# Kernel tuning notes

Hardware: AMD Instinct MI355X
Metric: run time of the kernel (lower is better)

## Reference

```python
import jax, jax.numpy as jnp
import numpy as np

N_NODES, N_EDGES, MAX_NB = 40000, 80000, 4
INPUT_SIZE, NODE_FDIM, HIDDEN = 384, 256, 256
DEPTH = 6


def setup_inputs() -> dict:
    key = jax.random.key(0)
    ks = jax.random.split(key, 16)
    s = 0.05  # weight init scale
    return {
        "fnode": jax.random.normal(ks[0], (N_NODES, NODE_FDIM), dtype=jnp.float32),
        "fmess": jax.random.normal(ks[1], (N_EDGES, INPUT_SIZE), dtype=jnp.float32),
        "agraph": jax.random.randint(ks[2], (N_NODES, MAX_NB), 0, N_EDGES),
        "bgraph": jax.random.randint(ks[3], (N_EDGES, MAX_NB), 0, N_EDGES),
        "mask": jnp.ones((N_NODES, 1), dtype=jnp.float32),
        "Wz": jax.random.normal(ks[4], (INPUT_SIZE + HIDDEN, HIDDEN), dtype=jnp.float32) * s,
        "bz": jnp.zeros((HIDDEN,), dtype=jnp.float32),
        "Wr": jax.random.normal(ks[5], (INPUT_SIZE, HIDDEN), dtype=jnp.float32) * s,
        "Ur": jax.random.normal(ks[6], (HIDDEN, HIDDEN), dtype=jnp.float32) * s,
        "bur": jnp.zeros((HIDDEN,), dtype=jnp.float32),
        "Wh": jax.random.normal(ks[7], (INPUT_SIZE + HIDDEN, HIDDEN), dtype=jnp.float32) * s,
        "bh": jnp.zeros((HIDDEN,), dtype=jnp.float32),
        "Wo": jax.random.normal(ks[8], (NODE_FDIM + HIDDEN, HIDDEN), dtype=jnp.float32) * s,
        "bo": jnp.zeros((HIDDEN,), dtype=jnp.float32),
        "depth": DEPTH,
    }


def reference(fnode, fmess, agraph, bgraph, mask, Wz, bz, Wr, Ur, bur, Wh, bh, Wo, bo, depth):
    E, H = fmess.shape[0], Wz.shape[1]
    # message 0 is padding -> kept at zero each step (mask[0,0]=0 in torch GRU)
    msg_mask = jnp.ones((E, 1), dtype=fmess.dtype).at[0, 0].set(0.0)
    rx = fmess @ Wr  # precomputable: [E, H], reset gate input term

    def step(h, _):
        h_nei = h[bgraph]                      # [E, nb, H] gather
        sum_h = h_nei.sum(axis=1)              # [E, H]
        z = jax.nn.sigmoid(jnp.concatenate([fmess, sum_h], axis=1) @ Wz + bz)
        r = jax.nn.sigmoid(rx[:, None, :] + h_nei @ Ur + bur)  # [E, nb, H]
        sum_gh = (r * h_nei).sum(axis=1)
        pre_h = jnp.tanh(jnp.concatenate([fmess, sum_gh], axis=1) @ Wh + bh)
        h_new = ((1.0 - z) * sum_h + z * pre_h) * msg_mask
        return h_new, None

    h0 = jnp.zeros((E, H), dtype=fmess.dtype)
    h, _ = jax.lax.scan(step, h0, None, length=depth)

    nei_message = h[agraph].sum(axis=1)        # [N, H] gather-sum over incoming edges
    node_hiddens = jax.nn.relu(jnp.concatenate([fnode, nei_message], axis=1) @ Wo + bo)
    return node_hiddens * mask, h
```

## Files before the change

kernel.cpp:

```cpp
#include <hip/hip_runtime.h>
#include <stdint.h>

#define N_NODES 40000
#define N_EDGES 80000
#define HID 256
#define DEPTH_FIXED 6
#define NPAD 40064

typedef __bf16 bf16;
typedef __bf16 bf16x4 __attribute__((ext_vector_type(4)));
typedef __bf16 bf16x8 __attribute__((ext_vector_type(8)));
typedef float f32x4 __attribute__((ext_vector_type(4)));

#define TPAD 136

__device__ __forceinline__ float sigmoidf_(float x) { return 1.f / (1.f + __expf(-x)); }
__device__ __forceinline__ float tanhf_(float x) { float e = __expf(2.f * x); return 1.f - 2.f / (e + 1.f); }

__device__ __forceinline__ void gld_lds16(const void* g, void* l) {
    __builtin_amdgcn_global_load_lds(
        (const __attribute__((address_space(1))) uint32_t*)g,
        (__attribute__((address_space(3))) uint32_t*)l, 16, 0, 0);
}

__device__ __forceinline__ void stage_tile(const bf16* __restrict__ src, int ld, int r0, int k0,
                                           bf16* lds, int tid) {
#pragma unroll
    for (int jj = 0; jj < 2; ++jj) {
        int s = jj * 256 + tid;
        int c = s ^ ((s >> 3) & 3);
        gld_lds16(src + (size_t)(r0 + (c >> 2)) * ld + k0 + (c & 3) * 8, lds + s * 8);
    }
}

__device__ __forceinline__ void mfma_tile(const bf16* lds_a, const bf16* lds_b,
                                          int wm, int wn, int lane, f32x4 (&acc)[4][4]) {
    const int li = lane & 15, quad = lane >> 4;
    const int sw = quad ^ ((li >> 1) & 3);
    bf16x8 a[4], b[4];
#pragma unroll
    for (int i = 0; i < 4; ++i)
        a[i] = *(const bf16x8*)(lds_a + ((wm * 64 + i * 16 + li) * 4 + sw) * 8);
#pragma unroll
    for (int j = 0; j < 4; ++j)
        b[j] = *(const bf16x8*)(lds_b + ((wn * 64 + j * 16 + li) * 4 + sw) * 8);
#pragma unroll
    for (int i = 0; i < 4; ++i)
#pragma unroll
        for (int j = 0; j < 4; ++j)
            acc[i][j] = __builtin_amdgcn_mfma_f32_16x16x32_bf16(a[i], b[j], acc[i][j], 0, 0, 0);
}

__global__ __launch_bounds__(256) void gemm_single_k(
    const bf16* __restrict__ A, const bf16* __restrict__ BT,
    const float* __restrict__ bias, bf16* __restrict__ C, int K, int ldc) {
    __shared__ __align__(16) char smem[34816];
    bf16* sA = (bf16*)smem;
    bf16* sB = sA + 4096;
    const int tid = threadIdx.x, lane = tid & 63, wave = tid >> 6;
    const int wm = wave >> 1, wn = wave & 1;
    const int m0 = blockIdx.x * 128, n0 = blockIdx.y * 128;
    f32x4 acc[4][4] = {};
    for (int k0 = 0; k0 < K; k0 += 32) {
        stage_tile(A, K, m0, k0, sA, tid);
        stage_tile(BT, K, n0, k0, sB, tid);
        __syncthreads();
        mfma_tile(sA, sB, wm, wn, lane, acc);
        __syncthreads();
    }
    bf16* tC = (bf16*)smem;
#pragma unroll
    for (int i = 0; i < 4; ++i)
#pragma unroll
        for (int j = 0; j < 4; ++j) {
            const int col = wn * 64 + j * 16 + (lane & 15);
#pragma unroll
            for (int r = 0; r < 4; ++r) {
                const int lr = wm * 64 + i * 16 + (lane >> 4) * 4 + r;
                tC[lr * TPAD + col] = (bf16)acc[i][j][r];
            }
        }
    __syncthreads();
#pragma unroll
    for (int s = 0; s < 8; ++s) {
        int v = s * 256 + tid;
        int lr = v >> 4, c8 = (v & 15) * 8;
        bf16x8 cv = *(const bf16x8*)(tC + lr * TPAD + c8);
        bf16x8 o;
        if (bias) {
            float4 b0 = *(const float4*)(bias + n0 + c8);
            float4 b1 = *(const float4*)(bias + n0 + c8 + 4);
            o[0] = (bf16)((float)cv[0] + b0.x); o[1] = (bf16)((float)cv[1] + b0.y);
            o[2] = (bf16)((float)cv[2] + b0.z); o[3] = (bf16)((float)cv[3] + b0.w);
            o[4] = (bf16)((float)cv[4] + b1.x); o[5] = (bf16)((float)cv[5] + b1.y);
            o[6] = (bf16)((float)cv[6] + b1.z); o[7] = (bf16)((float)cv[7] + b1.w);
        } else {
            o = cv;
        }
        *(bf16x8*)(C + (size_t)(m0 + lr) * ldc + n0 + c8) = o;
    }
}

__global__ __launch_bounds__(256) void gemm_gru_k(
    const bf16* __restrict__ A1, const bf16* __restrict__ A2,
    const bf16* __restrict__ B1T, const bf16* __restrict__ B2T,
    const bf16* __restrict__ P, bf16* __restrict__ H, float* __restrict__ HF) {
    __shared__ __align__(16) char smem[34816];
    bf16* s0 = (bf16*)smem;
    bf16* s1 = s0 + 4096;
    bf16* s2 = s1 + 4096;
    bf16* s3 = s2 + 4096;
    const int tid = threadIdx.x, lane = tid & 63, wave = tid >> 6;
    const int wm = wave >> 1, wn = wave & 1;
    const int m0 = blockIdx.x * 128, n0 = blockIdx.y * 128;
    f32x4 acc1[4][4] = {}, acc2[4][4] = {};
    for (int k0 = 0; k0 < 256; k0 += 32) {
        stage_tile(A1, 256, m0, k0, s0, tid);
        stage_tile(B1T, 256, n0, k0, s1, tid);
        stage_tile(A2, 256, m0, k0, s2, tid);
        stage_tile(B2T, 256, n0, k0, s3, tid);
        __syncthreads();
        mfma_tile(s0, s1, wm, wn, lane, acc1);
        mfma_tile(s2, s3, wm, wn, lane, acc2);
        __syncthreads();
    }
    bf16* tZ = (bf16*)smem;
    bf16* tH = tZ + 64 * TPAD;
#pragma unroll
    for (int pass = 0; pass < 2; ++pass) {
        if (wm == pass) {
#pragma unroll
            for (int i = 0; i < 4; ++i)
#pragma unroll
                for (int j = 0; j < 4; ++j) {
                    const int col = wn * 64 + j * 16 + (lane & 15);
#pragma unroll
                    for (int r = 0; r < 4; ++r) {
                        const int lr = i * 16 + (lane >> 4) * 4 + r;
                        tZ[lr * TPAD + col] = (bf16)acc1[i][j][r];
                        tH[lr * TPAD + col] = (bf16)acc2[i][j][r];
                    }
                }
        }
        __syncthreads();
#pragma unroll
        for (int s = 0; s < 4; ++s) {
            int v = s * 256 + tid;
            int lr = v >> 4, c8 = (v & 15) * 8;
            int grow = m0 + pass * 64 + lr;
            int gcol = n0 + c8;
            bf16x8 zl = *(const bf16x8*)(tZ + lr * TPAD + c8);
            bf16x8 hl = *(const bf16x8*)(tH + lr * TPAD + c8);
            bf16x8 zx = *(const bf16x8*)(P + (size_t)grow * 768 + 256 + gcol);
            bf16x8 hx = *(const bf16x8*)(P + (size_t)grow * 768 + 512 + gcol);
            bf16x8 sh = *(const bf16x8*)(A1 + (size_t)grow * 256 + gcol);
            bf16x8 o;
            float of[8];
#pragma unroll
            for (int r = 0; r < 8; ++r) {
                float z = sigmoidf_((float)zl[r] + (float)zx[r]);
                float p = tanhf_((float)hl[r] + (float)hx[r]);
                float hn = (1.f - z) * (float)sh[r] + z * p;
                if (grow == 0) hn = 0.f;
                o[r] = (bf16)hn;
                of[r] = hn;
            }
            *(bf16x8*)(H + (size_t)grow * 256 + gcol) = o;
            if (HF) {
                *(float4*)(HF + (size_t)grow * 256 + gcol) = make_float4(of[0], of[1], of[2], of[3]);
                *(float4*)(HF + (size_t)grow * 256 + gcol + 4) = make_float4(of[4], of[5], of[6], of[7]);
            }
        }
        __syncthreads();
    }
}

__global__ __launch_bounds__(256) void gemm_out_k(
    const bf16* __restrict__ A1, const bf16* __restrict__ A2,
    const bf16* __restrict__ B1T, const bf16* __restrict__ B2T,
    const float* __restrict__ bo, const float* __restrict__ mask, float* __restrict__ out) {
    __shared__ __align__(16) char smem[34816];
    bf16* s0 = (bf16*)smem;
    bf16* s1 = s0 + 4096;
    bf16* s2 = s1 + 4096;
    bf16* s3 = s2 + 4096;
    const int tid = threadIdx.x, lane = tid & 63, wave = tid >> 6;
    const int wm = wave >> 1, wn = wave & 1;
    const int m0 = blockIdx.x * 128, n0 = blockIdx.y * 128;
    f32x4 acc1[4][4] = {}, acc2[4][4] = {};
    for (int k0 = 0; k0 < 256; k0 += 32) {
        stage_tile(A1, 256, m0, k0, s0, tid);
        stage_tile(B1T, 256, n0, k0, s1, tid);
        stage_tile(A2, 256, m0, k0, s2, tid);
        stage_tile(B2T, 256, n0, k0, s3, tid);
        __syncthreads();
        mfma_tile(s0, s1, wm, wn, lane, acc1);
        mfma_tile(s2, s3, wm, wn, lane, acc2);
        __syncthreads();
    }
    bf16* tC = (bf16*)smem;
#pragma unroll
    for (int i = 0; i < 4; ++i)
#pragma unroll
        for (int j = 0; j < 4; ++j) {
            const int col = wn * 64 + j * 16 + (lane & 15);
#pragma unroll
            for (int r = 0; r < 4; ++r) {
                const int lr = wm * 64 + i * 16 + (lane >> 4) * 4 + r;
                tC[lr * TPAD + col] = (bf16)(acc1[i][j][r] + acc2[i][j][r]);
            }
        }
    __syncthreads();
#pragma unroll
    for (int s = 0; s < 8; ++s) {
        int v = s * 256 + tid;
        int lr = v >> 4, c8 = (v & 15) * 8;
        int grow = m0 + lr;
        if (grow >= N_NODES) continue;
        int gcol = n0 + c8;
        bf16x8 cv = *(const bf16x8*)(tC + lr * TPAD + c8);
        float4 b0 = *(const float4*)(bo + gcol);
        float4 b1 = *(const float4*)(bo + gcol + 4);
        float mk = mask[grow];
        float4 o0, o1;
        o0.x = fmaxf((float)cv[0] + b0.x, 0.f) * mk;
        o0.y = fmaxf((float)cv[1] + b0.y, 0.f) * mk;
        o0.z = fmaxf((float)cv[2] + b0.z, 0.f) * mk;
        o0.w = fmaxf((float)cv[3] + b0.w, 0.f) * mk;
        o1.x = fmaxf((float)cv[4] + b1.x, 0.f) * mk;
        o1.y = fmaxf((float)cv[5] + b1.y, 0.f) * mk;
        o1.z = fmaxf((float)cv[6] + b1.z, 0.f) * mk;
        o1.w = fmaxf((float)cv[7] + b1.w, 0.f) * mk;
        *(float4*)(out + (size_t)grow * 256 + gcol) = o0;
        *(float4*)(out + (size_t)grow * 256 + gcol + 4) = o1;
    }
}

__global__ __launch_bounds__(256) void gather_gru_k(
    const int* __restrict__ bgraph, const bf16* __restrict__ H, const bf16* __restrict__ HU,
    const bf16* __restrict__ P, bf16* __restrict__ sumH, bf16* __restrict__ sumGH) {
    int i = blockIdx.x * 256 + threadIdx.x;
    int e = i >> 5, c8 = (i & 31) * 8;
    int4 nb = *(const int4*)(bgraph + (size_t)e * 4);
    bf16x8 rx = *(const bf16x8*)(P + (size_t)e * 768 + c8);
    int bi[4] = {nb.x, nb.y, nb.z, nb.w};
    float sh[8] = {}, gh[8] = {};
#pragma unroll
    for (int j = 0; j < 4; ++j) {
        bf16x8 hv = *(const bf16x8*)(H + (size_t)bi[j] * HID + c8);
        bf16x8 uv = *(const bf16x8*)(HU + (size_t)bi[j] * HID + c8);
#pragma unroll
        for (int r = 0; r < 8; ++r) {
            float hf = (float)hv[r];
            float rr = sigmoidf_((float)rx[r] + (float)uv[r]);
            sh[r] += hf;
            gh[r] += rr * hf;
        }
    }
    bf16x8 os, og;
#pragma unroll
    for (int r = 0; r < 8; ++r) { os[r] = (bf16)sh[r]; og[r] = (bf16)gh[r]; }
    *(bf16x8*)(sumH + (size_t)e * HID + c8) = os;
    *(bf16x8*)(sumGH + (size_t)e * HID + c8) = og;
}

__global__ __launch_bounds__(256) void gather_nei_k(
    const int* __restrict__ agraph, const bf16* __restrict__ H, bf16* __restrict__ nei) {
    int i = blockIdx.x * 256 + threadIdx.x;
    int v = i >> 5, c8 = (i & 31) * 8;
    bf16x8 o;
    if (v < N_NODES) {
        int4 nb = *(const int4*)(agraph + (size_t)v * 4);
        int bi[4] = {nb.x, nb.y, nb.z, nb.w};
        float s[8] = {};
#pragma unroll
        for (int j = 0; j < 4; ++j) {
            bf16x8 hv = *(const bf16x8*)(H + (size_t)bi[j] * HID + c8);
#pragma unroll
            for (int r = 0; r < 8; ++r) s[r] += (float)hv[r];
        }
#pragma unroll
        for (int r = 0; r < 8; ++r) o[r] = (bf16)s[r];
    } else {
#pragma unroll
        for (int r = 0; r < 8; ++r) o[r] = (bf16)0.f;
    }
    *(bf16x8*)(nei + (size_t)v * HID + c8) = o;
}

__global__ __launch_bounds__(256) void step1_k(const bf16* __restrict__ P, bf16* __restrict__ H) {
    int i = blockIdx.x * 256 + threadIdx.x;
    int e = i >> 5, c8 = (i & 31) * 8;
    bf16x8 zx = *(const bf16x8*)(P + (size_t)e * 768 + 256 + c8);
    bf16x8 hx = *(const bf16x8*)(P + (size_t)e * 768 + 512 + c8);
    bf16x8 o;
#pragma unroll
    for (int r = 0; r < 8; ++r) {
        float h = sigmoidf_((float)zx[r]) * tanhf_((float)hx[r]);
        if (e == 0) h = 0.f;
        o[r] = (bf16)h;
    }
    *(bf16x8*)(H + (size_t)e * HID + c8) = o;
}

__global__ void cvt_bf16_k(const float* __restrict__ src, bf16* __restrict__ dst, int n4) {
    int i = blockIdx.x * 256 + threadIdx.x;
    if (i >= n4) return;
    float4 v = ((const float4*)src)[i];
    bf16x4 o = {(bf16)v.x, (bf16)v.y, (bf16)v.z, (bf16)v.w};
    *((bf16x4*)dst + i) = o;
}

__global__ void cvt_fnode_k(const float* __restrict__ src, bf16* __restrict__ dst) {
    int i = blockIdx.x * 256 + threadIdx.x;
    int row = i >> 6;
    bf16x4 o = {(bf16)0.f, (bf16)0.f, (bf16)0.f, (bf16)0.f};
    if (row < N_NODES) {
        float4 v = ((const float4*)src)[i];
        o[0] = (bf16)v.x; o[1] = (bf16)v.y; o[2] = (bf16)v.z; o[3] = (bf16)v.w;
    }
    *((bf16x4*)dst + i) = o;
}

__global__ void prep_wpre_k(const float* __restrict__ Wr, const float* __restrict__ Wz,
                            const float* __restrict__ Wh, bf16* __restrict__ WT) {
    int idx = blockIdx.x * 256 + threadIdx.x;
    if (idx >= 768 * 384) return;
    int n = idx / 384, k = idx % 384;
    float v;
    if (n < 256) v = Wr[(size_t)k * 256 + n];
    else if (n < 512) v = Wz[(size_t)k * 256 + (n - 256)];
    else v = Wh[(size_t)k * 256 + (n - 512)];
    WT[idx] = (bf16)v;
}

__global__ void prep_bias_k(const float* __restrict__ bur, const float* __restrict__ bz,
                            const float* __restrict__ bh, float* __restrict__ bp) {
    int n = blockIdx.x * 256 + threadIdx.x;
    if (n >= 768) return;
    bp[n] = n < 256 ? bur[n] : (n < 512 ? bz[n - 256] : bh[n - 512]);
}

__global__ void prep_t256_k(const float* __restrict__ W, bf16* __restrict__ T, int roff) {
    int idx = blockIdx.x * 256 + threadIdx.x;
    int n = idx >> 8, k = idx & 255;
    T[idx] = (bf16)W[(size_t)(roff + k) * 256 + n];
}

extern "C" void kernel_launch(void* const* d_in, const int* in_sizes, int n_in,
                              void* d_out, int out_size, void* d_ws, size_t ws_size,
                              hipStream_t stream) {
    (void)in_sizes; (void)n_in; (void)out_size; (void)ws_size;
    const float* fnode = (const float*)d_in[0];
    const float* fmess = (const float*)d_in[1];
    const int* agraph = (const int*)d_in[2];
    const int* bgraph = (const int*)d_in[3];
    const float* mask = (const float*)d_in[4];
    const float* Wz = (const float*)d_in[5];
    const float* bz = (const float*)d_in[6];
    const float* Wr = (const float*)d_in[7];
    const float* Ur = (const float*)d_in[8];
    const float* bur = (const float*)d_in[9];
    const float* Wh = (const float*)d_in[10];
    const float* bh = (const float*)d_in[11];
    const float* Wo = (const float*)d_in[12];
    const float* bo = (const float*)d_in[13];
    float* out_node = (float*)d_out;
    float* out_h = out_node + (size_t)N_NODES * HID;

    char* ws = (char*)d_ws;
    size_t off = 0;
    auto alloc = [&](size_t b) -> char* { char* p = ws + off; off += (b + 255) & ~(size_t)255; return p; };
    bf16* P     = (bf16*)alloc((size_t)N_EDGES * 768 * 2);
    bf16* Hb    = (bf16*)alloc((size_t)N_EDGES * HID * 2);
    bf16* HU    = (bf16*)alloc((size_t)N_EDGES * HID * 2);
    bf16* sumH  = (bf16*)alloc((size_t)N_EDGES * HID * 2);
    bf16* sumGH = (bf16*)alloc((size_t)N_EDGES * HID * 2);
    bf16* fnodeB= (bf16*)alloc((size_t)NPAD * HID * 2);
    bf16* nei   = (bf16*)alloc((size_t)NPAD * HID * 2);
    bf16* WTpre = (bf16*)alloc((size_t)768 * 384 * 2);
    bf16* UrT   = (bf16*)alloc(65536 * 2);
    bf16* WzBT  = (bf16*)alloc(65536 * 2);
    bf16* WhBT  = (bf16*)alloc(65536 * 2);
    bf16* WoTT  = (bf16*)alloc(65536 * 2);
    bf16* WoBT  = (bf16*)alloc(65536 * 2);
    float* biasP= (float*)alloc(768 * 4);
    bf16* fmessB = sumH;

    cvt_bf16_k<<<30000, 256, 0, stream>>>(fmess, fmessB, N_EDGES * 384 / 4);
    cvt_fnode_k<<<NPAD * 64 / 256, 256, 0, stream>>>(fnode, fnodeB);
    prep_wpre_k<<<(768 * 384 + 255) / 256, 256, 0, stream>>>(Wr, Wz, Wh, WTpre);
    prep_bias_k<<<3, 256, 0, stream>>>(bur, bz, bh, biasP);
    prep_t256_k<<<256, 256, 0, stream>>>(Ur, UrT, 0);
    prep_t256_k<<<256, 256, 0, stream>>>(Wz, WzBT, 384);
    prep_t256_k<<<256, 256, 0, stream>>>(Wh, WhBT, 384);
    prep_t256_k<<<256, 256, 0, stream>>>(Wo, WoTT, 0);
    prep_t256_k<<<256, 256, 0, stream>>>(Wo, WoBT, 256);

    gemm_single_k<<<dim3(625, 6), 256, 0, stream>>>(fmessB, WTpre, biasP, P, 384, 768);

    step1_k<<<N_EDGES * 32 / 256, 256, 0, stream>>>(P, Hb);

    for (int d = 2; d <= DEPTH_FIXED; ++d) {
        gemm_single_k<<<dim3(625, 2), 256, 0, stream>>>(Hb, UrT, nullptr, HU, 256, 256);
        gather_gru_k<<<N_EDGES * 32 / 256, 256, 0, stream>>>(bgraph, Hb, HU, P, sumH, sumGH);
        gemm_gru_k<<<dim3(625, 2), 256, 0, stream>>>(sumH, sumGH, WzBT, WhBT, P, Hb,
                                                     d == DEPTH_FIXED ? out_h : nullptr);
    }

    gather_nei_k<<<NPAD * 32 / 256, 256, 0, stream>>>(agraph, Hb, nei);
    gemm_out_k<<<dim3(313, 2), 256, 0, stream>>>(fnodeB, nei, WoTT, WoBT, bo, mask, out_node);
}
```

Baseline: 1.478 ms.

## Fuse neighbor gather-GRU with Z/H gate GEMM into one per-step kernel

Replaces the separate gather_gru kernel and the gate GEMM with one kernel that gathers neighbor messages for a 32-edge tile, keeps sum_h and gated sum in LDS, and runs both 256-wide GEMMs plus the GRU epilogue before writing the new hidden state. This removes the global write and re-read of the sumH/sumGH intermediates and one launch per step. To avoid read/write races it double-buffers the hidden state. The cost is a small M tile (32 rows), so every block restages the full weight matrices from global/L2, and the MFMA work per weight load is lower.

```diff
diff --git a/kernel.cpp b/kernel.cpp
--- a/kernel.cpp
+++ b/kernel.cpp
@@ -6,6 +6,7 @@
 #define HID 256
 #define DEPTH_FIXED 6
 #define NPAD 40064
+#define MT 32
 
 typedef __bf16 bf16;
 typedef __bf16 bf16x4 __attribute__((ext_vector_type(4)));
@@ -13,6 +14,7 @@
 typedef float f32x4 __attribute__((ext_vector_type(4)));
 
 #define TPAD 136
+#define APAD 264
 
 __device__ __forceinline__ float sigmoidf_(float x) { return 1.f / (1.f + __expf(-x)); }
 __device__ __forceinline__ float tanhf_(float x) { float e = __expf(2.f * x); return 1.f - 2.f / (e + 1.f); }
@@ -49,6 +51,132 @@
 #pragma unroll
         for (int j = 0; j < 4; ++j)
             acc[i][j] = __builtin_amdgcn_mfma_f32_16x16x32_bf16(a[i], b[j], acc[i][j], 0, 0, 0);
+}
+
+__global__ __launch_bounds__(256, 3) void step_fused_k(
+    const int* __restrict__ bgraph, const bf16* __restrict__ Hcur,
+    const bf16* __restrict__ HU, const bf16* __restrict__ P,
+    const bf16* __restrict__ B1T, const bf16* __restrict__ B2T,
+    bf16* __restrict__ Hnew, float* __restrict__ HF) {
+    __shared__ __align__(16) bf16 sA1[MT * APAD];
+    __shared__ __align__(16) bf16 sA2[MT * APAD];
+    __shared__ __align__(16) bf16 sBst[256 * 32];
+    const int tid = threadIdx.x, lane = tid & 63, wave = tid >> 6;
+    const int m0 = blockIdx.x * MT;
+
+    {
+        const int r = tid >> 3, qc = tid & 7;
+        const int e = m0 + r;
+        const int4 nb = *(const int4*)(bgraph + (size_t)e * 4);
+        const int bi[4] = {nb.x, nb.y, nb.z, nb.w};
+        const bf16* prx = P + (size_t)e * 768 + qc * 32;
+        bf16x8 rx[4];
+#pragma unroll
+        for (int c = 0; c < 4; ++c) rx[c] = *(const bf16x8*)(prx + c * 8);
+        float sh[4][8] = {}, gh[4][8] = {};
+#pragma unroll
+        for (int j = 0; j < 4; ++j) {
+            const bf16* hp = Hcur + (size_t)bi[j] * HID + qc * 32;
+            const bf16* up = HU + (size_t)bi[j] * HID + qc * 32;
+            bf16x8 hv[4], uv[4];
+#pragma unroll
+            for (int c = 0; c < 4; ++c) { hv[c] = *(const bf16x8*)(hp + c * 8); uv[c] = *(const bf16x8*)(up + c * 8); }
+#pragma unroll
+            for (int c = 0; c < 4; ++c)
+#pragma unroll
+                for (int u = 0; u < 8; ++u) {
+                    float hf = (float)hv[c][u];
+                    float rr = sigmoidf_((float)rx[c][u] + (float)uv[c][u]);
+                    sh[c][u] += hf;
+                    gh[c][u] += rr * hf;
+                }
+        }
+#pragma unroll
+        for (int c = 0; c < 4; ++c) {
+            bf16x8 os, og;
+#pragma unroll
+            for (int u = 0; u < 8; ++u) { os[u] = (bf16)sh[c][u]; og[u] = (bf16)gh[c][u]; }
+            *(bf16x8*)(sA1 + r * APAD + qc * 32 + c * 8) = os;
+            *(bf16x8*)(sA2 + r * APAD + qc * 32 + c * 8) = og;
+        }
+    }
+    __syncthreads();
+
+    const int li = lane & 15, quad = lane >> 4;
+    const int sw = quad ^ ((li >> 1) & 3);
+    f32x4 accZ[2][4] = {}, accH[2][4] = {};
+#pragma unroll
+    for (int pass = 0; pass < 2; ++pass) {
+        const bf16* BT = pass ? B2T : B1T;
+        const bf16* sA = pass ? sA2 : sA1;
+        for (int t = 0; t < 8; ++t) {
+#pragma unroll
+            for (int jj = 0; jj < 4; ++jj) {
+                int s = jj * 256 + tid;
+                int c = s ^ ((s >> 3) & 3);
+                gld_lds16(BT + (size_t)(c >> 2) * 256 + t * 32 + (c & 3) * 8, sBst + s * 8);
+            }
+            __syncthreads();
+            bf16x8 a[2], b[4];
+#pragma unroll
+            for (int i = 0; i < 2; ++i)
+                a[i] = *(const bf16x8*)(sA + (i * 16 + li) * APAD + t * 32 + quad * 8);
+#pragma unroll
+            for (int j = 0; j < 4; ++j)
+                b[j] = *(const bf16x8*)(sBst + ((wave * 64 + j * 16 + li) * 4 + sw) * 8);
+#pragma unroll
+            for (int i = 0; i < 2; ++i)
+#pragma unroll
+                for (int j = 0; j < 4; ++j) {
+                    if (pass == 0) accZ[i][j] = __builtin_amdgcn_mfma_f32_16x16x32_bf16(a[i], b[j], accZ[i][j], 0, 0, 0);
+                    else           accH[i][j] = __builtin_amdgcn_mfma_f32_16x16x32_bf16(a[i], b[j], accH[i][j], 0, 0, 0);
+                }
+            __syncthreads();
+        }
+    }
+
+    bf16* tZ = sA2;
+    bf16* tH = sBst;
+#pragma unroll
+    for (int i = 0; i < 2; ++i)
+#pragma unroll
+        for (int j = 0; j < 4; ++j) {
+            const int col = wave * 64 + j * 16 + li;
+#pragma unroll
+            for (int r = 0; r < 4; ++r) {
+                const int row = i * 16 + quad * 4 + r;
+                tZ[row * APAD + col] = (bf16)accZ[i][j][r];
+                tH[row * 256 + col] = (bf16)accH[i][j][r];
+            }
+        }
+    __syncthreads();
+#pragma unroll
+    for (int s = 0; s < 4; ++s) {
+        int v = s * 256 + tid;
+        int lr = v >> 5, c8 = (v & 31) * 8;
+        int e = m0 + lr;
+        bf16x8 zl = *(const bf16x8*)(tZ + lr * APAD + c8);
+        bf16x8 hl = *(const bf16x8*)(tH + lr * 256 + c8);
+        bf16x8 shv = *(const bf16x8*)(sA1 + lr * APAD + c8);
+        bf16x8 zx = *(const bf16x8*)(P + (size_t)e * 768 + 256 + c8);
+        bf16x8 hx = *(const bf16x8*)(P + (size_t)e * 768 + 512 + c8);
+        bf16x8 o;
+        float of[8];
+#pragma unroll
+        for (int u = 0; u < 8; ++u) {
+            float z = sigmoidf_((float)zl[u] + (float)zx[u]);
+            float p = tanhf_((float)hl[u] + (float)hx[u]);
+            float hn = (1.f - z) * (float)shv[u] + z * p;
+            if (e == 0) hn = 0.f;
+            o[u] = (bf16)hn;
+            of[u] = hn;
+        }
+        *(bf16x8*)(Hnew + (size_t)e * HID + c8) = o;
+        if (HF) {
+            *(float4*)(HF + (size_t)e * HID + c8) = make_float4(of[0], of[1], of[2], of[3]);
+            *(float4*)(HF + (size_t)e * HID + c8 + 4) = make_float4(of[4], of[5], of[6], of[7]);
+        }
+    }
 }
 
 __global__ __launch_bounds__(256) void gemm_single_k(
@@ -98,80 +226,6 @@
             o = cv;
         }
         *(bf16x8*)(C + (size_t)(m0 + lr) * ldc + n0 + c8) = o;
-    }
-}
-
-__global__ __launch_bounds__(256) void gemm_gru_k(
-    const bf16* __restrict__ A1, const bf16* __restrict__ A2,
-    const bf16* __restrict__ B1T, const bf16* __restrict__ B2T,
-    const bf16* __restrict__ P, bf16* __restrict__ H, float* __restrict__ HF) {
-    __shared__ __align__(16) char smem[34816];
-    bf16* s0 = (bf16*)smem;
-    bf16* s1 = s0 + 4096;
-    bf16* s2 = s1 + 4096;
-    bf16* s3 = s2 + 4096;
-    const int tid = threadIdx.x, lane = tid & 63, wave = tid >> 6;
-    const int wm = wave >> 1, wn = wave & 1;
-    const int m0 = blockIdx.x * 128, n0 = blockIdx.y * 128;
-    f32x4 acc1[4][4] = {}, acc2[4][4] = {};
-    for (int k0 = 0; k0 < 256; k0 += 32) {
-        stage_tile(A1, 256, m0, k0, s0, tid);
-        stage_tile(B1T, 256, n0, k0, s1, tid);
-        stage_tile(A2, 256, m0, k0, s2, tid);
-        stage_tile(B2T, 256, n0, k0, s3, tid);
-        __syncthreads();
-        mfma_tile(s0, s1, wm, wn, lane, acc1);
-        mfma_tile(s2, s3, wm, wn, lane, acc2);
-        __syncthreads();
-    }
-    bf16* tZ = (bf16*)smem;
-    bf16* tH = tZ + 64 * TPAD;
-#pragma unroll
-    for (int pass = 0; pass < 2; ++pass) {
-        if (wm == pass) {
-#pragma unroll
-            for (int i = 0; i < 4; ++i)
-#pragma unroll
-                for (int j = 0; j < 4; ++j) {
-                    const int col = wn * 64 + j * 16 + (lane & 15);
-#pragma unroll
-                    for (int r = 0; r < 4; ++r) {
-                        const int lr = i * 16 + (lane >> 4) * 4 + r;
-                        tZ[lr * TPAD + col] = (bf16)acc1[i][j][r];
-                        tH[lr * TPAD + col] = (bf16)acc2[i][j][r];
-                    }
-                }
-        }
-        __syncthreads();
-#pragma unroll
-        for (int s = 0; s < 4; ++s) {
-            int v = s * 256 + tid;
-            int lr = v >> 4, c8 = (v & 15) * 8;
-            int grow = m0 + pass * 64 + lr;
-            int gcol = n0 + c8;
-            bf16x8 zl = *(const bf16x8*)(tZ + lr * TPAD + c8);
-            bf16x8 hl = *(const bf16x8*)(tH + lr * TPAD + c8);
-            bf16x8 zx = *(const bf16x8*)(P + (size_t)grow * 768 + 256 + gcol);
-            bf16x8 hx = *(const bf16x8*)(P + (size_t)grow * 768 + 512 + gcol);
-            bf16x8 sh = *(const bf16x8*)(A1 + (size_t)grow * 256 + gcol);
-            bf16x8 o;
-            float of[8];
-#pragma unroll
-            for (int r = 0; r < 8; ++r) {
-                float z = sigmoidf_((float)zl[r] + (float)zx[r]);
-                float p = tanhf_((float)hl[r] + (float)hx[r]);
-                float hn = (1.f - z) * (float)sh[r] + z * p;
-                if (grow == 0) hn = 0.f;
-                o[r] = (bf16)hn;
-                of[r] = hn;
-            }
-            *(bf16x8*)(H + (size_t)grow * 256 + gcol) = o;
-            if (HF) {
-                *(float4*)(HF + (size_t)grow * 256 + gcol) = make_float4(of[0], of[1], of[2], of[3]);
-                *(float4*)(HF + (size_t)grow * 256 + gcol + 4) = make_float4(of[4], of[5], of[6], of[7]);
-            }
-        }
-        __syncthreads();
     }
 }
 
@@ -236,34 +290,6 @@
     }
 }
 
-__global__ __launch_bounds__(256) void gather_gru_k(
-    const int* __restrict__ bgraph, const bf16* __restrict__ H, const bf16* __restrict__ HU,
-    const bf16* __restrict__ P, bf16* __restrict__ sumH, bf16* __restrict__ sumGH) {
-    int i = blockIdx.x * 256 + threadIdx.x;
-    int e = i >> 5, c8 = (i & 31) * 8;
-    int4 nb = *(const int4*)(bgraph + (size_t)e * 4);
-    bf16x8 rx = *(const bf16x8*)(P + (size_t)e * 768 + c8);
-    int bi[4] = {nb.x, nb.y, nb.z, nb.w};
-    float sh[8] = {}, gh[8] = {};
-#pragma unroll
-    for (int j = 0; j < 4; ++j) {
-        bf16x8 hv = *(const bf16x8*)(H + (size_t)bi[j] * HID + c8);
-        bf16x8 uv = *(const bf16x8*)(HU + (size_t)bi[j] * HID + c8);
-#pragma unroll
-        for (int r = 0; r < 8; ++r) {
-            float hf = (float)hv[r];
-            float rr = sigmoidf_((float)rx[r] + (float)uv[r]);
-            sh[r] += hf;
-            gh[r] += rr * hf;
-        }
-    }
-    bf16x8 os, og;
-#pragma unroll
-    for (int r = 0; r < 8; ++r) { os[r] = (bf16)sh[r]; og[r] = (bf16)gh[r]; }
-    *(bf16x8*)(sumH + (size_t)e * HID + c8) = os;
-    *(bf16x8*)(sumGH + (size_t)e * HID + c8) = og;
-}
-
 __global__ __launch_bounds__(256) void gather_nei_k(
     const int* __restrict__ agraph, const bf16* __restrict__ H, bf16* __restrict__ nei) {
     int i = blockIdx.x * 256 + threadIdx.x;
@@ -372,10 +398,9 @@
     size_t off = 0;
     auto alloc = [&](size_t b) -> char* { char* p = ws + off; off += (b + 255) & ~(size_t)255; return p; };
     bf16* P     = (bf16*)alloc((size_t)N_EDGES * 768 * 2);
-    bf16* Hb    = (bf16*)alloc((size_t)N_EDGES * HID * 2);
+    bf16* Hb0   = (bf16*)alloc((size_t)N_EDGES * HID * 2);
+    bf16* Hb1   = (bf16*)alloc((size_t)N_EDGES * HID * 2);
     bf16* HU    = (bf16*)alloc((size_t)N_EDGES * HID * 2);
-    bf16* sumH  = (bf16*)alloc((size_t)N_EDGES * HID * 2);
-    bf16* sumGH = (bf16*)alloc((size_t)N_EDGES * HID * 2);
     bf16* fnodeB= (bf16*)alloc((size_t)NPAD * HID * 2);
     bf16* nei   = (bf16*)alloc((size_t)NPAD * HID * 2);
     bf16* WTpre = (bf16*)alloc((size_t)768 * 384 * 2);
@@ -385,7 +410,7 @@
     bf16* WoTT  = (bf16*)alloc(65536 * 2);
     bf16* WoBT  = (bf16*)alloc(65536 * 2);
     float* biasP= (float*)alloc(768 * 4);
-    bf16* fmessB = sumH;
+    bf16* fmessB = Hb1;
 
     cvt_bf16_k<<<30000, 256, 0, stream>>>(fmess, fmessB, N_EDGES * 384 / 4);
     cvt_fnode_k<<<NPAD * 64 / 256, 256, 0, stream>>>(fnode, fnodeB);
@@ -399,15 +424,17 @@
 
     gemm_single_k<<<dim3(625, 6), 256, 0, stream>>>(fmessB, WTpre, biasP, P, 384, 768);
 
-    step1_k<<<N_EDGES * 32 / 256, 256, 0, stream>>>(P, Hb);
-
+    step1_k<<<N_EDGES * 32 / 256, 256, 0, stream>>>(P, Hb0);
+
+    bf16* cur = Hb0;
+    bf16* nxt = Hb1;
     for (int d = 2; d <= DEPTH_FIXED; ++d) {
-        gemm_single_k<<<dim3(625, 2), 256, 0, stream>>>(Hb, UrT, nullptr, HU, 256, 256);
-        gather_gru_k<<<N_EDGES * 32 / 256, 256, 0, stream>>>(bgraph, Hb, HU, P, sumH, sumGH);
-        gemm_gru_k<<<dim3(625, 2), 256, 0, stream>>>(sumH, sumGH, WzBT, WhBT, P, Hb,
-                                                     d == DEPTH_FIXED ? out_h : nullptr);
-    }
-
-    gather_nei_k<<<NPAD * 32 / 256, 256, 0, stream>>>(agraph, Hb, nei);
+        gemm_single_k<<<dim3(625, 2), 256, 0, stream>>>(cur, UrT, nullptr, HU, 256, 256);
+        step_fused_k<<<N_EDGES / MT, 256, 0, stream>>>(bgraph, cur, HU, P, WzBT, WhBT, nxt,
+                                                       d == DEPTH_FIXED ? out_h : nullptr);
+        bf16* t = cur; cur = nxt; nxt = t;
+    }
+
+    gather_nei_k<<<NPAD * 32 / 256, 256, 0, stream>>>(agraph, cur, nei);
     gemm_out_k<<<dim3(313, 2), 256, 0, stream>>>(fnodeB, nei, WoTT, WoBT, bo, mask, out_node);
 }
```

Result: faster. 1.395 ms (-5.7%).
